# Kernel optimization log

Measured on AMD Instinct MI355X. Metric: run time of the kernel, lower is better.

Reference implementation:

```python
import jax, jax.numpy as jnp
import numpy as np

B, S, T, E, H, V = 32, 64, 64, 512, 512, 32000  # batch, src len, tgt len, embed, hidden(per dir), vocab


def _lstm_scan(xs, Wih, Whh, bih, bhh, h0, c0):
    # xs: [S, B, E]; PyTorch gate order i, f, g, o
    def step(carry, x):
        h, c = carry
        g = x @ Wih.T + bih + h @ Whh.T + bhh
        i, f, gg, o = jnp.split(g, 4, axis=-1)
        c = jax.nn.sigmoid(f) * c + jax.nn.sigmoid(i) * jnp.tanh(gg)
        h = jax.nn.sigmoid(o) * jnp.tanh(c)
        return (h, c), h
    (hT, cT), hs = jax.lax.scan(step, (h0, c0), xs)
    return hs, hT, cT


def setup_inputs() -> dict:
    key = jax.random.key(0)
    ks = jax.random.split(key, 20)
    p = lambda k, shape, s=0.05: (jax.random.normal(k, shape, jnp.float32) * s)
    inp = {
        "input_chunk": jax.random.randint(ks[0], (B, S), 0, V),
        "target_chunk": jax.random.randint(ks[1], (B, T), 0, V),
        "enc_emb": jax.random.uniform(ks[2], (V, E), jnp.float32, -0.1, 0.1),
        "dec_emb": jax.random.uniform(ks[3], (V, E), jnp.float32, -0.1, 0.1),
        # encoder bidirectional LSTM (1 layer)
        "Wih_f": p(ks[4], (4 * H, E)), "Whh_f": p(ks[5], (4 * H, H)),
        "bih_f": p(ks[6], (4 * H,)), "bhh_f": p(ks[7], (4 * H,)),
        "Wih_b": p(ks[8], (4 * H, E)), "Whh_b": p(ks[9], (4 * H, H)),
        "bih_b": p(ks[10], (4 * H,)), "bhh_b": p(ks[11], (4 * H,)),
        # decoder LSTMCell: input 2H+E, hidden 2H
        "Wih_d": p(ks[12], (8 * H, 2 * H + E)), "Whh_d": p(ks[13], (8 * H, 2 * H)),
        "bih_d": p(ks[14], (8 * H,)), "bhh_d": p(ks[15], (8 * H,)),
        # attention projection 2H -> 2H
        "Wa": p(ks[16], (2 * H, 2 * H)), "ba": p(ks[17], (2 * H,)),
        # output projection 2H -> V (bias initialized to 0 in the module)
        "Wout": p(ks[18], (V, 2 * H)), "bout": jnp.zeros((V,), jnp.float32),
    }
    return inp


def reference(input_chunk, target_chunk, enc_emb, dec_emb,
              Wih_f, Whh_f, bih_f, bhh_f, Wih_b, Whh_b, bih_b, bhh_b,
              Wih_d, Whh_d, bih_d, bhh_d, Wa, ba, Wout, bout):
    # ---- Encoder: bidirectional LSTM ----
    x = enc_emb[input_chunk]                 # [B, S, E]
    xs = jnp.transpose(x, (1, 0, 2))         # [S, B, E]
    h0 = jnp.zeros((B, H), x.dtype)
    c0 = jnp.zeros((B, H), x.dtype)
    hs_f, hT_f, cT_f = _lstm_scan(xs, Wih_f, Whh_f, bih_f, bhh_f, h0, c0)
    hs_b, hT_b, cT_b = _lstm_scan(xs[::-1], Wih_b, Whh_b, bih_b, bhh_b, h0, c0)
    hs_b = hs_b[::-1]
    all_hidden = jnp.concatenate([hs_f, hs_b], axis=-1)          # [S, B, 2H]
    all_hidden = jnp.transpose(all_hidden, (1, 0, 2))            # [B, S, 2H]
    dec_h = jnp.concatenate([hT_f, hT_b], axis=-1)               # [B, 2H]
    dec_c = jnp.concatenate([cT_f, cT_b], axis=-1)               # [B, 2H]

    # ---- Decoder: attention + LSTMCell loop (teacher forcing = 1.0, no dropout) ----
    A = all_hidden @ Wa.T + ba               # W_attention(all_hidden), constant across steps
    tgt_emb = dec_emb[target_chunk]          # [B, T, E]
    # feed at t=0 is zeros; afterwards the t-th target embedding
    feeds = jnp.concatenate([jnp.zeros((B, 1, E), tgt_emb.dtype), tgt_emb[:, :-1]], axis=1)
    feeds = jnp.transpose(feeds, (1, 0, 2))  # [T, B, E]

    def dstep(carry, feed):
        h, c = carry
        scores = jnp.einsum('bsd,bd->bs', A, h)                  # [B, S]
        attn = jax.nn.softmax(scores, axis=1)
        ctx = jnp.einsum('bs,bsd->bd', attn, all_hidden)         # [B, 2H]
        inp = jnp.concatenate([ctx, feed], axis=1)               # [B, 2H+E]
        g = inp @ Wih_d.T + bih_d + h @ Whh_d.T + bhh_d
        i, f, gg, o = jnp.split(g, 4, axis=-1)
        c = jax.nn.sigmoid(f) * c + jax.nn.sigmoid(i) * jnp.tanh(gg)
        h = jax.nn.sigmoid(o) * jnp.tanh(c)
        logits = h @ Wout.T + bout                               # [B, V]
        return (h, c), logits

    _, logits = jax.lax.scan(dstep, (dec_h, dec_c), feeds)       # [T, B, V]
    logits = jnp.transpose(logits, (1, 0, 2))                    # [B, T, V]
    outputs = jnp.argmax(logits, axis=-1)                        # [B, T]
    return logits, outputs
```

## Files before the change

### kernel.cpp

```cpp
#include <hip/hip_runtime.h>
#include <hip/hip_bf16.h>

#define BB 32
#define SS 64
#define TT 64
#define EE 512
#define HH 512
#define VV 32000

#define O_C0    0u
#define O_C1    32768u
#define O_HD    65536u
#define O_CD    98304u
#define O_PENC  131072u
#define O_PDEC  655360u
#define O_CTX   1179648u
#define O_ALLH  1212416u
#define O_AATT  3309568u
#define O_HDEC  5406720u
#define O_PACK  7503872u
#define O_DA1   7507968u
#define O_DA2   7540736u
#define O_W1    7573504u
#define WS_NEED 95830016ull

#define S_GXF   0u
#define S_GXB   4194304u
#define S_GFEED 8388608u
#define U_BASE  17000000u

typedef float f32x4 __attribute__((ext_vector_type(4)));
typedef _Float16 f16x8 __attribute__((ext_vector_type(8)));
typedef _Float16 f16x4 __attribute__((ext_vector_type(4)));

__device__ __forceinline__ float sigm_(float x){ return 1.0f/(1.0f + expf(-x)); }

__device__ __forceinline__ unsigned int fkey_(float f){
  unsigned int u = __float_as_uint(f);
  return (u & 0x80000000u) ? ~u : (u | 0x80000000u);
}

__device__ __forceinline__ int swz_(int row, int kb){
  return (row*64 + kb) ^ ((row & 7) << 4);
}
__device__ __forceinline__ int swz128_(int row, int kb){
  return (row*128 + kb) ^ ((row & 7) << 4);
}

__global__ __launch_bounds__(256) void k_init(float* __restrict__ ws){
  int i = blockIdx.x*256 + threadIdx.x;
  if (i < 65536) ws[i] = 0.0f;
  if (i < 2048) ((unsigned long long*)(ws + O_PACK))[i] = 0ull;
}

__global__ __launch_bounds__(256) void k_cvtW(
    const float* __restrict__ Whh_f, const float* __restrict__ Whh_b,
    const float* __restrict__ Wih_d, const float* __restrict__ Whh_d,
    _Float16* __restrict__ dst)
{
  int g = blockIdx.x*256 + threadIdx.x;
  int idx = g*4;
  f32x4 v;
  if (idx < 1048576){
    v = *(const f32x4*)(Whh_f + idx);
  } else if (idx < 2097152){
    v = *(const f32x4*)(Whh_b + (idx - 1048576));
  } else {
    int j = idx - 2097152;
    int row = j >> 11, col = j & 2047;
    const float* src = (col < 1024) ? (Wih_d + (size_t)row*1536 + col)
                                    : (Whh_d + (size_t)row*1024 + (col - 1024));
    v = *(const f32x4*)src;
  }
  f16x4 h;
  #pragma unroll
  for (int c = 0; c < 4; ++c) h[c] = (_Float16)v[c];
  *(f16x4*)(dst + idx) = h;
}

__global__ __launch_bounds__(256) void k_cvtWout(
    const float* __restrict__ Wout, _Float16* __restrict__ W1)
{
  size_t i = ((size_t)blockIdx.x*256 + threadIdx.x)*8;
  f32x4 x0 = *(const f32x4*)(Wout + i);
  f32x4 x1 = *(const f32x4*)(Wout + i + 4);
  f16x4 h0, h1;
  #pragma unroll
  for (int c = 0; c < 4; ++c){ h0[c] = (_Float16)x0[c]; h1[c] = (_Float16)x1[c]; }
  *(f16x4*)(W1 + i)   = h0;
  *(f16x4*)(W1 + i+4) = h1;
}

template<int MODE>
__global__ __launch_bounds__(256) void k_gemm(
    const float* __restrict__ A, int lda,
    const int* __restrict__ chunk,
    const float* __restrict__ W, int ldW,
    const float* __restrict__ bias0, const float* __restrict__ bias1,
    float* __restrict__ C, int ldC, int K)
{
  __shared__ float As[16*68];
  __shared__ float Bs[16*68];
  int tid = threadIdx.x;
  int n0 = blockIdx.x*64, m0 = blockIdx.y*64;
  int tx = tid & 15, ty = tid >> 4;
  int lrow = tid >> 2, kq = tid & 3;

  const float* arp;
  if (MODE == 0) {
    arp = A + (size_t)(m0 + lrow)*lda;
  } else if (MODE == 1) {
    int m = m0 + lrow; int s = m >> 5, b = m & 31;
    arp = A + (size_t)chunk[b*SS + s]*EE;
  } else {
    int m = m0 + lrow; int t = m >> 5, b = m & 31;
    arp = (t == 0) ? nullptr : A + (size_t)chunk[b*TT + (t-1)]*EE;
  }
  const float* wrp = W + (size_t)(n0 + lrow)*ldW;

  float acc[4][4] = {};
  for (int k0 = 0; k0 < K; k0 += 16){
    float4 va = make_float4(0.f,0.f,0.f,0.f);
    if (MODE == 0) va = *(const float4*)&arp[k0 + kq*4];
    else if (arp)  va = *(const float4*)&arp[k0 + kq*4];
    float4 vw = *(const float4*)&wrp[k0 + kq*4];
    As[(kq*4+0)*68 + lrow] = va.x;
    As[(kq*4+1)*68 + lrow] = va.y;
    As[(kq*4+2)*68 + lrow] = va.z;
    As[(kq*4+3)*68 + lrow] = va.w;
    Bs[(kq*4+0)*68 + lrow] = vw.x;
    Bs[(kq*4+1)*68 + lrow] = vw.y;
    Bs[(kq*4+2)*68 + lrow] = vw.z;
    Bs[(kq*4+3)*68 + lrow] = vw.w;
    __syncthreads();
    #pragma unroll
    for (int kk = 0; kk < 16; ++kk){
      float4 a4 = *(const float4*)&As[kk*68 + ty*4];
      float4 b4 = *(const float4*)&Bs[kk*68 + tx*4];
      float av[4] = {a4.x,a4.y,a4.z,a4.w};
      float bv[4] = {b4.x,b4.y,b4.z,b4.w};
      #pragma unroll
      for (int i=0;i<4;++i)
        #pragma unroll
        for (int j=0;j<4;++j)
          acc[i][j] = fmaf(av[i], bv[j], acc[i][j]);
    }
    __syncthreads();
  }
  float bv[4];
  #pragma unroll
  for (int j = 0; j < 4; ++j){
    int n = n0 + tx*4 + j;
    float bb = 0.f;
    if (bias0) bb += bias0[n];
    if (bias1) bb += bias1[n];
    bv[j] = bb;
  }
  #pragma unroll
  for (int i = 0; i < 4; ++i){
    int m = m0 + ty*4 + i;
    float4 v = make_float4(acc[i][0]+bv[0], acc[i][1]+bv[1], acc[i][2]+bv[2], acc[i][3]+bv[3]);
    *(float4*)&C[(size_t)m*ldC + n0 + tx*4] = v;
  }
}

__global__ __launch_bounds__(256) void k_enc_step(
    const _Float16* __restrict__ wenc,
    float* __restrict__ ws, const float* __restrict__ oscr, int t)
{
  __shared__ float hl[128*36];
  __shared__ float Wt[32*132];
  int sub = blockIdx.x, kp = blockIdx.y, dir = blockIdx.z;
  int tid = threadIdx.x;
  int s = dir ? (63 - t) : t;
  int p = t & 1;
  const float* gx  = oscr + (dir ? S_GXB : S_GXF);
  const float* prd = ws + (p ? O_PDEC : O_PENC) + dir*262144u;
  const float* cin = ws + O_C0 + p*32768u + dir*16384u;
  float* cout = ws + O_C0 + (p^1)*32768u + dir*16384u;

  {
    int ug = tid & 31, bg = tid >> 5;
    int ul0 = ug*4;
    int u0 = kp*128 + ul0;
    #pragma unroll
    for (int j = 0; j < 4; ++j){
      int b = bg*4 + j;
      size_t gbase = (size_t)(s*32 + b)*2048u;
      f32x4 g0 = *(const f32x4*)&gx[gbase + u0];
      f32x4 g1 = *(const f32x4*)&gx[gbase + 512 + u0];
      f32x4 g2 = *(const f32x4*)&gx[gbase + 1024 + u0];
      f32x4 g3 = *(const f32x4*)&gx[gbase + 1536 + u0];
      if (t > 0){
        #pragma unroll
        for (int kq = 0; kq < 4; ++kq){
          const float* pp = prd + kq*65536u + (size_t)b*2048u;
          g0 += *(const f32x4*)&pp[u0];
          g1 += *(const f32x4*)&pp[512 + u0];
          g2 += *(const f32x4*)&pp[1024 + u0];
          g3 += *(const f32x4*)&pp[1536 + u0];
        }
      }
      f32x4 c = *(const f32x4*)&cin[b*512 + u0];
      f32x4 cn, hn;
      #pragma unroll
      for (int e = 0; e < 4; ++e){
        float cc = sigm_(g1[e])*c[e] + sigm_(g0[e])*tanhf(g2[e]);
        float hh = sigm_(g3[e])*tanhf(cc);
        cn[e] = cc; hn[e] = hh;
        hl[(ul0+e)*36 + b] = hh;
      }
      if (sub == 0){
        *(f32x4*)&cout[b*512 + u0] = cn;
        *(f32x4*)&ws[O_ALLH + (size_t)(b*64 + s)*1024u + dir*512 + u0] = hn;
      }
    }
  }
  __syncthreads();
  if (t == 63) return;

  const _Float16* W = wenc + dir*1048576u;
  float* P = ws + (p ? O_PENC : O_PDEC) + dir*262144u + kp*65536u;
  int rg2 = tid & 31, bg2 = tid >> 5;
  int wrow = tid & 127, whalf = tid >> 7;
  float acc[4][4] = {};
  for (int kt = 0; kt < 4; ++kt){
    #pragma unroll
    for (int i = 0; i < 4; ++i){
      int chunk = whalf*4 + i;
      int grow = sub*128 + wrow;
      f16x4 v = *(const f16x4*)&W[(size_t)grow*512 + kp*128 + kt*32 + chunk*4];
      Wt[(chunk*4+0)*132 + wrow] = (float)v[0];
      Wt[(chunk*4+1)*132 + wrow] = (float)v[1];
      Wt[(chunk*4+2)*132 + wrow] = (float)v[2];
      Wt[(chunk*4+3)*132 + wrow] = (float)v[3];
    }
    __syncthreads();
    #pragma unroll 8
    for (int kk = 0; kk < 32; ++kk){
      f32x4 wv = *(const f32x4*)&Wt[kk*132 + rg2*4];
      f32x4 hv = *(const f32x4*)&hl[(kt*32+kk)*36 + bg2*4];
      #pragma unroll
      for (int i = 0; i < 4; ++i)
        #pragma unroll
        for (int j = 0; j < 4; ++j)
          acc[i][j] = fmaf(wv[i], hv[j], acc[i][j]);
    }
    __syncthreads();
  }
  #pragma unroll
  for (int j = 0; j < 4; ++j){
    int b = bg2*4 + j;
    f32x4 v; v[0]=acc[0][j]; v[1]=acc[1][j]; v[2]=acc[2][j]; v[3]=acc[3][j];
    *(f32x4*)&P[(size_t)b*2048u + sub*128 + rg2*4] = v;
  }
}

__global__ __launch_bounds__(256) void k_concat(float* __restrict__ ws){
  int i = blockIdx.x*256 + threadIdx.x;
  int which = i >> 15;
  int idx = i & 32767;
  int b = idx >> 10, u = idx & 1023;
  int dir = (u >= 512);
  int uu = u & 511;
  float v;
  if (which == 0){
    int s = dir ? 0 : 63;
    v = ws[O_ALLH + (size_t)(b*64 + s)*1024u + u];
  } else {
    v = ws[O_C0 + dir*16384u + b*512 + uu];
  }
  ws[(which ? O_CD : O_HD) + b*1024 + u] = v;
}

__global__ __launch_bounds__(256) void k_attn(float* __restrict__ ws,
                                              const float* __restrict__ oscr, int t){
  __shared__ float hlq[1024];
  __shared__ float part[64][5];
  __shared__ float sc[64];
  __shared__ float atn[64];
  __shared__ float dsh;
  int b = blockIdx.x, tid = threadIdx.x;
  float* hd = ws + O_HD;
  float* cd = ws + O_CD;
  float* G  = ws + O_PDEC;
  _Float16* DA1 = (_Float16*)(ws + O_DA1);
  _Float16* DA2 = (_Float16*)(ws + O_DA2);
  if (t > 0){
    const float* gfd = oscr + S_GFEED + (size_t)((t-1)*32 + b)*4096u;
    for (int u = tid; u < 1024; u += 256){
      float g0 = gfd[u]      + G[(size_t)b*4096u + u];
      float g1 = gfd[1024+u] + G[(size_t)b*4096u + 1024 + u];
      float g2 = gfd[2048+u] + G[(size_t)b*4096u + 2048 + u];
      float g3 = gfd[3072+u] + G[(size_t)b*4096u + 3072 + u];
      float c = cd[b*1024 + u];
      c = sigm_(g1)*c + sigm_(g0)*tanhf(g2);
      float h = sigm_(g3)*tanhf(c);
      cd[b*1024+u] = c; hd[b*1024+u] = h; hlq[u] = h;
      ws[O_HDEC + (size_t)(b*64 + (t-1))*1024u + u] = h;
      _Float16 hi = (_Float16)h;
      DA1[(size_t)b*2048u + 1024 + u] = hi;
      DA2[(size_t)b*2048u + 1024 + u] = (_Float16)((h - (float)hi)*2048.0f);
    }
  } else {
    for (int u = tid; u < 1024; u += 256){
      float h = hd[b*1024 + u];
      hlq[u] = h;
      _Float16 hi = (_Float16)h;
      DA1[(size_t)b*2048u + 1024 + u] = hi;
      DA2[(size_t)b*2048u + 1024 + u] = (_Float16)((h - (float)hi)*2048.0f);
    }
  }
  __syncthreads();
  {
    int s = tid >> 2, p = tid & 3;
    const float* Ar = ws + O_AATT + (size_t)(b*64 + s)*1024u + p*256;
    const float* hp = &hlq[p*256];
    float sum = 0.f;
    #pragma unroll 8
    for (int k4 = 0; k4 < 64; ++k4){
      float4 a = *(const float4*)&Ar[k4*4];
      float4 h4 = *(const float4*)&hp[k4*4];
      sum = fmaf(a.x,h4.x, fmaf(a.y,h4.y, fmaf(a.z,h4.z, fmaf(a.w,h4.w, sum))));
    }
    part[s][p] = sum;
  }
  __syncthreads();
  if (tid < 64) sc[tid] = part[tid][0] + part[tid][1] + part[tid][2] + part[tid][3];
  __syncthreads();
  if (tid < 64){
    float m = sc[0];
    #pragma unroll
    for (int i = 1; i < 64; ++i) m = fmaxf(m, sc[i]);
    atn[tid] = expf(sc[tid] - m);
  }
  __syncthreads();
  if (tid == 0){
    float d = 0.f;
    #pragma unroll
    for (int i = 0; i < 64; ++i) d += atn[i];
    dsh = 1.0f/d;
  }
  __syncthreads();
  {
    float rd = dsh;
    float ax=0.f, ay=0.f, az=0.f, aw=0.f;
    const float* ah = ws + O_ALLH + (size_t)(b*64)*1024u + tid*4;
    for (int s2 = 0; s2 < 64; ++s2){
      float a = atn[s2];
      float4 v = *(const float4*)&ah[(size_t)s2*1024u];
      ax = fmaf(a, v.x, ax); ay = fmaf(a, v.y, ay);
      az = fmaf(a, v.z, az); aw = fmaf(a, v.w, aw);
    }
    float o[4] = {ax*rd, ay*rd, az*rd, aw*rd};
    #pragma unroll
    for (int j = 0; j < 4; ++j){
      int u = tid*4 + j;
      _Float16 hi = (_Float16)o[j];
      DA1[(size_t)b*2048u + u] = hi;
      DA2[(size_t)b*2048u + u] = (_Float16)((o[j] - (float)hi)*2048.0f);
    }
  }
}

__global__ __launch_bounds__(256) void k_dec_gemm(
    const _Float16* __restrict__ wdec, float* __restrict__ ws)
{
  __shared__ char glds[24576];
  int bid = blockIdx.x, tid = threadIdx.x;
  float* G = ws + O_PDEC;
  const _Float16* DA1 = (const _Float16*)(ws + O_DA1);
  const _Float16* DA2 = (const _Float16*)(ws + O_DA2);
  const float rs = 1.0f/2048.0f;
  int lane = tid & 63, w = tid >> 6;
  int lr = lane & 15, lg = lane >> 4;
  int mfw = w >> 1, nfw = w & 1;
  int arow = tid >> 3, aseg = tid & 7;
  const _Float16* a1src = DA1 + (size_t)arow*2048u + aseg*8;
  const _Float16* a2src = DA2 + (size_t)arow*2048u + aseg*8;
  const _Float16* wsrc  = wdec + (size_t)(bid*32 + arow)*2048u + aseg*8;
  f32x4 accH, accM;
  accH[0]=accH[1]=accH[2]=accH[3]=0.f;
  accM[0]=accM[1]=accM[2]=accM[3]=0.f;
  uint4 rA1 = *(const uint4*)a1src;
  uint4 rA2 = *(const uint4*)a2src;
  uint4 rW  = *(const uint4*)wsrc;
  int so = swz128_(arow, aseg*16);
  int raA = swz128_(mfw*16 + lr, lg*16);
  int raW = swz128_(nfw*16 + lr, lg*16);
  for (int kt = 0; kt < 32; ++kt){
    char* base = glds + (kt & 1)*12288;
    char* A1t = base; char* A2t = base + 4096; char* Wt = base + 8192;
    *(uint4*)(A1t + so) = rA1;
    *(uint4*)(A2t + so) = rA2;
    *(uint4*)(Wt  + so) = rW;
    __syncthreads();
    if (kt < 31){
      int ko = (kt+1)*64;
      rA1 = *(const uint4*)(a1src + ko);
      rA2 = *(const uint4*)(a2src + ko);
      rW  = *(const uint4*)(wsrc + ko);
    }
    #pragma unroll
    for (int ks = 0; ks < 2; ++ks){
      f16x8 a1 = *(const f16x8*)(A1t + (raA ^ (ks*64)));
      f16x8 a2 = *(const f16x8*)(A2t + (raA ^ (ks*64)));
      f16x8 wf = *(const f16x8*)(Wt  + (raW ^ (ks*64)));
      accH = __builtin_amdgcn_mfma_f32_16x16x32_f16(a1, wf, accH, 0, 0, 0);
      accM = __builtin_amdgcn_mfma_f32_16x16x32_f16(a2, wf, accM, 0, 0, 0);
    }
    __syncthreads();
  }
  #pragma unroll
  for (int r = 0; r < 4; ++r){
    int b = mfw*16 + lg*4 + r;
    int n = bid*32 + nfw*16 + lr;
    G[(size_t)b*4096u + n] = accH[r] + accM[r]*rs;
  }
}

__global__ __launch_bounds__(256) void k_dec_pw_last(float* __restrict__ ws,
                                                     const float* __restrict__ oscr){
  int g = blockIdx.x*256 + threadIdx.x;
  int b = g >> 10, u = g & 1023;
  const float* gfd = oscr + S_GFEED + (size_t)(63*32 + b)*4096u;
  const float* G = ws + O_PDEC;
  float g0 = gfd[u]      + G[(size_t)b*4096u + u];
  float g1 = gfd[1024+u] + G[(size_t)b*4096u + 1024 + u];
  float g2 = gfd[2048+u] + G[(size_t)b*4096u + 2048 + u];
  float g3 = gfd[3072+u] + G[(size_t)b*4096u + 3072 + u];
  float c = ws[O_CD + b*1024 + u];
  c = sigm_(g1)*c + sigm_(g0)*tanhf(g2);
  float h = sigm_(g3)*tanhf(c);
  ws[O_HDEC + (size_t)(b*64 + 63)*1024u + u] = h;
}

__global__ __launch_bounds__(256) void k_cvtA(float* __restrict__ ws){
  const float* src = ws + O_HDEC;
  _Float16* A1 = (_Float16*)(ws + O_ALLH);
  _Float16* A2 = (_Float16*)(ws + O_AATT);
  int i = (blockIdx.x*256 + threadIdx.x)*8;
  f32x4 x0 = *(const f32x4*)&src[i];
  f32x4 x1 = *(const f32x4*)&src[i+4];
  f16x4 h0, h1, l0, l1;
  #pragma unroll
  for (int c = 0; c < 4; ++c){
    _Float16 a = (_Float16)x0[c];
    h0[c] = a; l0[c] = (_Float16)((x0[c] - (float)a)*2048.0f);
    _Float16 bq = (_Float16)x1[c];
    h1[c] = bq; l1[c] = (_Float16)((x1[c] - (float)bq)*2048.0f);
  }
  *(f16x4*)&A1[i]   = h0;
  *(f16x4*)&A1[i+4] = h1;
  *(f16x4*)&A2[i]   = l0;
  *(f16x4*)&A2[i+4] = l1;
}

__global__ __launch_bounds__(256) void k_logits(
    const _Float16* __restrict__ A1, const _Float16* __restrict__ A2,
    const _Float16* __restrict__ W1, const float* __restrict__ bout,
    float* __restrict__ out, unsigned long long* __restrict__ pk)
{
  __shared__ char lds[49152];
  int tid = threadIdx.x;
  int n0 = blockIdx.y*128, m0 = blockIdx.x*128;
  int lane = tid & 63, wave = tid >> 6;
  int wm = wave >> 1, wn = wave & 1;
  int lr = lane & 15, lg = lane >> 4;

  int s0 = tid*2, s1 = tid*2 + 1;
  int ar0 = s0 >> 2, as0 = s0 & 3;
  int ar1 = s1 >> 2, as1 = s1 & 3;
  const _Float16* a1p0 = A1 + (size_t)(m0 + ar0)*1024u + as0*8;
  const _Float16* a1p1 = A1 + (size_t)(m0 + ar1)*1024u + as1*8;
  const _Float16* a2p0 = A2 + (size_t)(m0 + ar0)*1024u + as0*8;
  const _Float16* a2p1 = A2 + (size_t)(m0 + ar1)*1024u + as1*8;
  const _Float16* wp0  = W1 + (size_t)(n0 + ar0)*1024u + as0*8;
  const _Float16* wp1  = W1 + (size_t)(n0 + ar1)*1024u + as1*8;

  f32x4 accH[4][4], accM[4][4];
  #pragma unroll
  for (int i = 0; i < 4; ++i)
    #pragma unroll
    for (int j = 0; j < 4; ++j){
      f32x4 z; z[0]=z[1]=z[2]=z[3]=0.f;
      accH[i][j] = z; accM[i][j] = z;
    }

  uint4 r10, r11, r20, r21, rw0, rw1;
  r10 = *(const uint4*)a1p0; r11 = *(const uint4*)a1p1;
  r20 = *(const uint4*)a2p0; r21 = *(const uint4*)a2p1;
  rw0 = *(const uint4*)wp0;  rw1 = *(const uint4*)wp1;

  for (int kt = 0; kt < 32; ++kt){
    int cur = kt & 1;
    char* base = lds + cur*24576;
    char* A1t = base, *A2t = base + 8192, *Wt = base + 16384;
    *(uint4*)(A1t + swz_(ar0, as0*16)) = r10;
    *(uint4*)(A1t + swz_(ar1, as1*16)) = r11;
    *(uint4*)(A2t + swz_(ar0, as0*16)) = r20;
    *(uint4*)(A2t + swz_(ar1, as1*16)) = r21;
    *(uint4*)(Wt  + swz_(ar0, as0*16)) = rw0;
    *(uint4*)(Wt  + swz_(ar1, as1*16)) = rw1;
    __syncthreads();
    if (kt < 31){
      int ko = (kt+1)*32;
      r10 = *(const uint4*)(a1p0 + ko); r11 = *(const uint4*)(a1p1 + ko);
      r20 = *(const uint4*)(a2p0 + ko); r21 = *(const uint4*)(a2p1 + ko);
      rw0 = *(const uint4*)(wp0 + ko);  rw1 = *(const uint4*)(wp1 + ko);
    }
    f16x8 wf[4];
    #pragma unroll
    for (int nf = 0; nf < 4; ++nf)
      wf[nf] = *(const f16x8*)(Wt + swz_(wn*64 + nf*16 + lr, lg*16));
    #pragma unroll
    for (int mf = 0; mf < 4; ++mf){
      int ad = swz_(wm*64 + mf*16 + lr, lg*16);
      f16x8 a1f = *(const f16x8*)(A1t + ad);
      f16x8 a2f = *(const f16x8*)(A2t + ad);
      #pragma unroll
      for (int nf = 0; nf < 4; ++nf){
        accH[mf][nf] = __builtin_amdgcn_mfma_f32_16x16x32_f16(a1f, wf[nf], accH[mf][nf], 0, 0, 0);
        accM[mf][nf] = __builtin_amdgcn_mfma_f32_16x16x32_f16(a2f, wf[nf], accM[mf][nf], 0, 0, 0);
      }
    }
    __syncthreads();
  }

  const float rs = 1.0f/2048.0f;
  float bb[4];
  #pragma unroll
  for (int nf = 0; nf < 4; ++nf) bb[nf] = bout[n0 + wn*64 + nf*16 + lr];
  #pragma unroll
  for (int mf = 0; mf < 4; ++mf){
    #pragma unroll
    for (int r = 0; r < 4; ++r){
      int m = m0 + wm*64 + mf*16 + lg*4 + r;
      unsigned long long bk = 0ull;
      #pragma unroll
      for (int nf = 0; nf < 4; ++nf){
        int n = n0 + wn*64 + nf*16 + lr;
        float val = accH[mf][nf][r] + accM[mf][nf][r]*rs + bb[nf];
        __builtin_nontemporal_store(val, &out[(size_t)m*VV + n]);
        unsigned long long p = ((unsigned long long)fkey_(val) << 32) | (unsigned int)(~(unsigned int)n);
        if (p > bk) bk = p;
      }
      #pragma unroll
      for (int off = 1; off < 16; off <<= 1){
        unsigned long long o = __shfl_xor(bk, off, 64);
        if (o > bk) bk = o;
      }
      if (lr == 0) atomicMax(&pk[m], bk);
    }
  }
}

__global__ __launch_bounds__(512) void k_logits_fb(
    const _Float16* __restrict__ A1, const _Float16* __restrict__ A2,
    const float* __restrict__ Wout, const float* __restrict__ bout,
    float* __restrict__ out, unsigned long long* __restrict__ pk)
{
  __shared__ char lds[49152];
  char* A1t = lds;
  char* A2t = lds + 8192;
  char* W1t = lds + 16384;
  char* W2t = lds + 32768;
  int tid = threadIdx.x;
  int n0 = blockIdx.x*256;
  int lane = tid & 63, wave = tid >> 6;
  int wm = wave >> 2, wn = wave & 3;
  int lr = lane & 15, lg = lane >> 4;

  int arow = tid >> 2, aseg = tid & 3;
  int wrow = tid >> 1, wseg = tid & 1;
  const float* wp = Wout + (size_t)(n0 + wrow)*1024u + wseg*16;

  float bb[4];
  #pragma unroll
  for (int nf = 0; nf < 4; ++nf) bb[nf] = bout[n0 + wn*64 + nf*16 + lr];
  const float rs = 1.0f/2048.0f;

  for (int mi = 0; mi < 4; ++mi){
    int m0 = (blockIdx.y*4 + mi)*128;
    const _Float16* a1p = A1 + (size_t)(m0 + arow)*1024u + aseg*8;
    const _Float16* a2p = A2 + (size_t)(m0 + arow)*1024u + aseg*8;

    f32x4 accH[4][4], accM[4][4];
    #pragma unroll
    for (int i = 0; i < 4; ++i)
      #pragma unroll
      for (int j = 0; j < 4; ++j){
        f32x4 z; z[0]=z[1]=z[2]=z[3]=0.f;
        accH[i][j] = z; accM[i][j] = z;
      }

    for (int k0 = 0; k0 < 1024; k0 += 32){
      uint4 av1 = *(const uint4*)(a1p + k0);
      uint4 av2 = *(const uint4*)(a2p + k0);
      f32x4 wv[4];
      #pragma unroll
      for (int i = 0; i < 4; ++i) wv[i] = *(const f32x4*)(wp + k0 + i*4);
      __syncthreads();
      *(uint4*)(A1t + swz_(arow, aseg*16)) = av1;
      *(uint4*)(A2t + swz_(arow, aseg*16)) = av2;
      f16x8 hi[2], lo[2];
      #pragma unroll
      for (int i = 0; i < 2; ++i)
        #pragma unroll
        for (int c = 0; c < 8; ++c){
          float x = wv[i*2 + (c>>2)][c&3];
          _Float16 h = (_Float16)x;
          hi[i][c] = h;
          lo[i][c] = (_Float16)((x - (float)h)*2048.0f);
        }
      *(f16x8*)(W1t + swz_(wrow, wseg*32 +  0)) = hi[0];
      *(f16x8*)(W1t + swz_(wrow, wseg*32 + 16)) = hi[1];
      *(f16x8*)(W2t + swz_(wrow, wseg*32 +  0)) = lo[0];
      *(f16x8*)(W2t + swz_(wrow, wseg*32 + 16)) = lo[1];
      __syncthreads();
      f16x8 w1f[4], w2f[4];
      #pragma unroll
      for (int nf = 0; nf < 4; ++nf){
        int ad = swz_(wn*64 + nf*16 + lr, lg*16);
        w1f[nf] = *(const f16x8*)(W1t + ad);
        w2f[nf] = *(const f16x8*)(W2t + ad);
      }
      #pragma unroll
      for (int mf = 0; mf < 4; ++mf){
        int ad = swz_(wm*64 + mf*16 + lr, lg*16);
        f16x8 a1f = *(const f16x8*)(A1t + ad);
        f16x8 a2f = *(const f16x8*)(A2t + ad);
        #pragma unroll
        for (int nf = 0; nf < 4; ++nf){
          accH[mf][nf] = __builtin_amdgcn_mfma_f32_16x16x32_f16(a1f, w1f[nf], accH[mf][nf], 0, 0, 0);
          accM[mf][nf] = __builtin_amdgcn_mfma_f32_16x16x32_f16(a1f, w2f[nf], accM[mf][nf], 0, 0, 0);
          accM[mf][nf] = __builtin_amdgcn_mfma_f32_16x16x32_f16(a2f, w1f[nf], accM[mf][nf], 0, 0, 0);
        }
      }
    }

    #pragma unroll
    for (int mf = 0; mf < 4; ++mf){
      #pragma unroll
      for (int r = 0; r < 4; ++r){
        int m = m0 + wm*64 + mf*16 + lg*4 + r;
        unsigned long long bk = 0ull;
        #pragma unroll
        for (int nf = 0; nf < 4; ++nf){
          int n = n0 + wn*64 + nf*16 + lr;
          float val = accH[mf][nf][r] + accM[mf][nf][r]*rs + bb[nf];
          __builtin_nontemporal_store(val, &out[(size_t)m*VV + n]);
          unsigned long long p = ((unsigned long long)fkey_(val) << 32) | (unsigned int)(~(unsigned int)n);
          if (p > bk) bk = p;
        }
        #pragma unroll
        for (int off = 1; off < 16; off <<= 1){
          unsigned long long o = __shfl_xor(bk, off, 64);
          if (o > bk) bk = o;
        }
        if (lr == 0) atomicMax(&pk[m], bk);
      }
    }
  }
}

__global__ __launch_bounds__(256) void k_argmax(
    const unsigned long long* __restrict__ pk, float* __restrict__ out)
{
  int i = blockIdx.x*256 + threadIdx.x;
  if (i < 2048){
    unsigned int low = (unsigned int)(pk[i] & 0xFFFFFFFFull);
    unsigned int col = ~low;
    out[(size_t)BB*TT*VV + i] = (float)col;
  }
}

extern "C" void kernel_launch(void* const* d_in, const int* in_sizes, int n_in,
                              void* d_out, int out_size, void* d_ws, size_t ws_size,
                              hipStream_t stream)
{
  const int*   input_chunk  = (const int*)d_in[0];
  const int*   target_chunk = (const int*)d_in[1];
  const float* enc_emb = (const float*)d_in[2];
  const float* dec_emb = (const float*)d_in[3];
  const float* Wih_f = (const float*)d_in[4];
  const float* Whh_f = (const float*)d_in[5];
  const float* bih_f = (const float*)d_in[6];
  const float* bhh_f = (const float*)d_in[7];
  const float* Wih_b = (const float*)d_in[8];
  const float* Whh_b = (const float*)d_in[9];
  const float* bih_b = (const float*)d_in[10];
  const float* bhh_b = (const float*)d_in[11];
  const float* Wih_d = (const float*)d_in[12];
  const float* Whh_d = (const float*)d_in[13];
  const float* bih_d = (const float*)d_in[14];
  const float* bhh_d = (const float*)d_in[15];
  const float* Wa   = (const float*)d_in[16];
  const float* ba   = (const float*)d_in[17];
  const float* Wout = (const float*)d_in[18];
  const float* bout = (const float*)d_in[19];
  float* ws = (float*)d_ws;
  float* out = (float*)d_out;
  float* oscr = (float*)d_out;
  _Float16* wf16 = (_Float16*)(oscr + U_BASE);
  bool bigws = (ws_size >= WS_NEED);

  k_init<<<256, 256, 0, stream>>>(ws);
  k_cvtW<<<10240, 256, 0, stream>>>(Whh_f, Whh_b, Wih_d, Whh_d, wf16);
  if (bigws)
    k_cvtWout<<<16000, 256, 0, stream>>>(Wout, (_Float16*)(ws + O_W1));

  k_gemm<1><<<dim3(32,32), 256, 0, stream>>>(enc_emb, 512, input_chunk, Wih_f, 512, bih_f, bhh_f, oscr + S_GXF, 2048, 512);
  k_gemm<1><<<dim3(32,32), 256, 0, stream>>>(enc_emb, 512, input_chunk, Wih_b, 512, bih_b, bhh_b, oscr + S_GXB, 2048, 512);
  k_gemm<2><<<dim3(64,32), 256, 0, stream>>>(dec_emb, 512, target_chunk, Wih_d + 1024, 1536, bih_d, bhh_d, oscr + S_GFEED, 4096, 512);

  for (int t = 0; t < 64; ++t){
    k_enc_step<<<dim3(16,4,2), 256, 0, stream>>>(wf16, ws, oscr, t);
  }

  k_concat<<<256, 256, 0, stream>>>(ws);
  k_gemm<0><<<dim3(16,32), 256, 0, stream>>>(ws + O_ALLH, 1024, nullptr, Wa, 1024, ba, nullptr, ws + O_AATT, 1024, 1024);

  const _Float16* wdec = wf16 + 2097152u;
  for (int t = 0; t < 64; ++t){
    k_attn<<<32, 256, 0, stream>>>(ws, oscr, t);
    k_dec_gemm<<<128, 256, 0, stream>>>(wdec, ws);
  }
  k_dec_pw_last<<<128, 256, 0, stream>>>(ws, oscr);

  k_cvtA<<<1024, 256, 0, stream>>>(ws);
  if (bigws){
    k_logits<<<dim3(16,250), 256, 0, stream>>>(
        (const _Float16*)(ws + O_ALLH), (const _Float16*)(ws + O_AATT),
        (const _Float16*)(ws + O_W1), bout, out, (unsigned long long*)(ws + O_PACK));
  } else {
    k_logits_fb<<<dim3(125,4), 512, 0, stream>>>(
        (const _Float16*)(ws + O_ALLH), (const _Float16*)(ws + O_AATT),
        Wout, bout, out, (unsigned long long*)(ws + O_PACK));
  }
  k_argmax<<<8, 256, 0, stream>>>((const unsigned long long*)(ws + O_PACK), out);
}
```

Before: 4.064 ms.

## Move encoder recurrent GEMM to split-fp16 MFMA and drop LDS staging in decoder GEMM

```diff
diff --git a/kernel.cpp b/kernel.cpp
--- a/kernel.cpp
+++ b/kernel.cpp
@@ -9,7 +9,6 @@
 #define VV 32000
 
 #define O_C0    0u
-#define O_C1    32768u
 #define O_HD    65536u
 #define O_CD    98304u
 #define O_PENC  131072u
@@ -43,13 +42,10 @@
 __device__ __forceinline__ int swz_(int row, int kb){
   return (row*64 + kb) ^ ((row & 7) << 4);
 }
-__device__ __forceinline__ int swz128_(int row, int kb){
-  return (row*128 + kb) ^ ((row & 7) << 4);
-}
 
 __global__ __launch_bounds__(256) void k_init(float* __restrict__ ws){
   int i = blockIdx.x*256 + threadIdx.x;
-  if (i < 65536) ws[i] = 0.0f;
+  if (i < 131072) ws[i] = 0.0f;
   if (i < 2048) ((unsigned long long*)(ws + O_PACK))[i] = 0ull;
 }
 
@@ -168,92 +164,97 @@
     const _Float16* __restrict__ wenc,
     float* __restrict__ ws, const float* __restrict__ oscr, int t)
 {
-  __shared__ float hl[128*36];
-  __shared__ float Wt[32*132];
-  int sub = blockIdx.x, kp = blockIdx.y, dir = blockIdx.z;
+  __shared__ _Float16 hA1[32][520];
+  __shared__ _Float16 hA2[32][520];
+  int nb = blockIdx.x, dir = blockIdx.y;
   int tid = threadIdx.x;
   int s = dir ? (63 - t) : t;
   int p = t & 1;
   const float* gx  = oscr + (dir ? S_GXB : S_GXF);
-  const float* prd = ws + (p ? O_PDEC : O_PENC) + dir*262144u;
+  const float* Gin = ws + O_PENC + (size_t)(p*2 + dir)*65536u;
+  float* Gout      = ws + O_PENC + (size_t)((p^1)*2 + dir)*65536u;
   const float* cin = ws + O_C0 + p*32768u + dir*16384u;
-  float* cout = ws + O_C0 + (p^1)*32768u + dir*16384u;
-
-  {
-    int ug = tid & 31, bg = tid >> 5;
-    int ul0 = ug*4;
-    int u0 = kp*128 + ul0;
-    #pragma unroll
-    for (int j = 0; j < 4; ++j){
-      int b = bg*4 + j;
-      size_t gbase = (size_t)(s*32 + b)*2048u;
-      f32x4 g0 = *(const f32x4*)&gx[gbase + u0];
-      f32x4 g1 = *(const f32x4*)&gx[gbase + 512 + u0];
-      f32x4 g2 = *(const f32x4*)&gx[gbase + 1024 + u0];
-      f32x4 g3 = *(const f32x4*)&gx[gbase + 1536 + u0];
-      if (t > 0){
-        #pragma unroll
-        for (int kq = 0; kq < 4; ++kq){
-          const float* pp = prd + kq*65536u + (size_t)b*2048u;
-          g0 += *(const f32x4*)&pp[u0];
-          g1 += *(const f32x4*)&pp[512 + u0];
-          g2 += *(const f32x4*)&pp[1024 + u0];
-          g3 += *(const f32x4*)&pp[1536 + u0];
-        }
-      }
-      f32x4 c = *(const f32x4*)&cin[b*512 + u0];
-      f32x4 cn, hn;
-      #pragma unroll
-      for (int e = 0; e < 4; ++e){
-        float cc = sigm_(g1[e])*c[e] + sigm_(g0[e])*tanhf(g2[e]);
-        float hh = sigm_(g3[e])*tanhf(cc);
-        cn[e] = cc; hn[e] = hh;
-        hl[(ul0+e)*36 + b] = hh;
-      }
-      if (sub == 0){
-        *(f32x4*)&cout[b*512 + u0] = cn;
-        *(f32x4*)&ws[O_ALLH + (size_t)(b*64 + s)*1024u + dir*512 + u0] = hn;
-      }
+  float* cout      = ws + O_C0 + (p^1)*32768u + dir*16384u;
+
+  #pragma unroll
+  for (int j = 0; j < 16; ++j){
+    int item = tid + j*256;
+    int b = item >> 7, u0 = (item & 127)*4;
+    size_t gb = (size_t)(s*32 + b)*2048u + u0;
+    f32x4 g0 = *(const f32x4*)&gx[gb];
+    f32x4 g1 = *(const f32x4*)&gx[gb + 512];
+    f32x4 g2 = *(const f32x4*)&gx[gb + 1024];
+    f32x4 g3 = *(const f32x4*)&gx[gb + 1536];
+    if (t > 0){
+      int o = b*2048 + u0;
+      g0 += *(const f32x4*)&Gin[o];
+      g1 += *(const f32x4*)&Gin[o + 512];
+      g2 += *(const f32x4*)&Gin[o + 1024];
+      g3 += *(const f32x4*)&Gin[o + 1536];
+    }
+    f32x4 c = *(const f32x4*)&cin[b*512 + u0];
+    f32x4 cn, hn;
+    f16x4 h1v, h2v;
+    #pragma unroll
+    for (int e = 0; e < 4; ++e){
+      float cc = sigm_(g1[e])*c[e] + sigm_(g0[e])*tanhf(g2[e]);
+      float hh = sigm_(g3[e])*tanhf(cc);
+      cn[e] = cc; hn[e] = hh;
+      _Float16 hi = (_Float16)hh;
+      h1v[e] = hi;
+      h2v[e] = (_Float16)((hh - (float)hi)*2048.0f);
+    }
+    *(f16x4*)&hA1[b][u0] = h1v;
+    *(f16x4*)&hA2[b][u0] = h2v;
+    if (nb == 0){
+      *(f32x4*)&cout[b*512 + u0] = cn;
+      *(f32x4*)&ws[O_ALLH + (size_t)(b*64 + s)*1024u + dir*512 + u0] = hn;
     }
   }
   __syncthreads();
   if (t == 63) return;
 
-  const _Float16* W = wenc + dir*1048576u;
-  float* P = ws + (p ? O_PENC : O_PDEC) + dir*262144u + kp*65536u;
-  int rg2 = tid & 31, bg2 = tid >> 5;
-  int wrow = tid & 127, whalf = tid >> 7;
-  float acc[4][4] = {};
-  for (int kt = 0; kt < 4; ++kt){
-    #pragma unroll
-    for (int i = 0; i < 4; ++i){
-      int chunk = whalf*4 + i;
-      int grow = sub*128 + wrow;
-      f16x4 v = *(const f16x4*)&W[(size_t)grow*512 + kp*128 + kt*32 + chunk*4];
-      Wt[(chunk*4+0)*132 + wrow] = (float)v[0];
-      Wt[(chunk*4+1)*132 + wrow] = (float)v[1];
-      Wt[(chunk*4+2)*132 + wrow] = (float)v[2];
-      Wt[(chunk*4+3)*132 + wrow] = (float)v[3];
-    }
-    __syncthreads();
-    #pragma unroll 8
-    for (int kk = 0; kk < 32; ++kk){
-      f32x4 wv = *(const f32x4*)&Wt[kk*132 + rg2*4];
-      f32x4 hv = *(const f32x4*)&hl[(kt*32+kk)*36 + bg2*4];
-      #pragma unroll
-      for (int i = 0; i < 4; ++i)
-        #pragma unroll
-        for (int j = 0; j < 4; ++j)
-          acc[i][j] = fmaf(wv[i], hv[j], acc[i][j]);
-    }
-    __syncthreads();
-  }
-  #pragma unroll
-  for (int j = 0; j < 4; ++j){
-    int b = bg2*4 + j;
-    f32x4 v; v[0]=acc[0][j]; v[1]=acc[1][j]; v[2]=acc[2][j]; v[3]=acc[3][j];
-    *(f32x4*)&P[(size_t)b*2048u + sub*128 + rg2*4] = v;
-  }
+  const _Float16* W = wenc + (size_t)dir*1048576u;
+  int lane = tid & 63, w = tid >> 6;
+  int lr = lane & 15, lg = lane >> 4;
+  int n0g = nb*256 + w*64;
+  f32x4 accH[2][4], accM[2][4];
+  #pragma unroll
+  for (int i = 0; i < 2; ++i)
+    #pragma unroll
+    for (int j = 0; j < 4; ++j){
+      f32x4 z; z[0]=z[1]=z[2]=z[3]=0.f;
+      accH[i][j] = z; accM[i][j] = z;
+    }
+  for (int kt = 0; kt < 16; ++kt){
+    int koff = kt*32 + lg*8;
+    f16x8 a1f[2], a2f[2];
+    #pragma unroll
+    for (int mf = 0; mf < 2; ++mf){
+      a1f[mf] = *(const f16x8*)&hA1[mf*16 + lr][koff];
+      a2f[mf] = *(const f16x8*)&hA2[mf*16 + lr][koff];
+    }
+    #pragma unroll
+    for (int nf = 0; nf < 4; ++nf){
+      f16x8 wf = *(const f16x8*)&W[(size_t)(n0g + nf*16 + lr)*512u + koff];
+      #pragma unroll
+      for (int mf = 0; mf < 2; ++mf){
+        accH[mf][nf] = __builtin_amdgcn_mfma_f32_16x16x32_f16(a1f[mf], wf, accH[mf][nf], 0, 0, 0);
+        accM[mf][nf] = __builtin_amdgcn_mfma_f32_16x16x32_f16(a2f[mf], wf, accM[mf][nf], 0, 0, 0);
+      }
+    }
+  }
+  const float rs = 1.0f/2048.0f;
+  #pragma unroll
+  for (int mf = 0; mf < 2; ++mf)
+    #pragma unroll
+    for (int nf = 0; nf < 4; ++nf)
+      #pragma unroll
+      for (int r = 0; r < 4; ++r){
+        int b = mf*16 + lg*4 + r;
+        int n = n0g + nf*16 + lr;
+        Gout[b*2048 + n] = accH[mf][nf][r] + accM[mf][nf][r]*rs;
+      }
 }
 
 __global__ __launch_bounds__(256) void k_concat(float* __restrict__ ws){
@@ -366,55 +367,33 @@
 __global__ __launch_bounds__(256) void k_dec_gemm(
     const _Float16* __restrict__ wdec, float* __restrict__ ws)
 {
-  __shared__ char glds[24576];
   int bid = blockIdx.x, tid = threadIdx.x;
   float* G = ws + O_PDEC;
   const _Float16* DA1 = (const _Float16*)(ws + O_DA1);
   const _Float16* DA2 = (const _Float16*)(ws + O_DA2);
-  const float rs = 1.0f/2048.0f;
   int lane = tid & 63, w = tid >> 6;
   int lr = lane & 15, lg = lane >> 4;
-  int mfw = w >> 1, nfw = w & 1;
-  int arow = tid >> 3, aseg = tid & 7;
-  const _Float16* a1src = DA1 + (size_t)arow*2048u + aseg*8;
-  const _Float16* a2src = DA2 + (size_t)arow*2048u + aseg*8;
-  const _Float16* wsrc  = wdec + (size_t)(bid*32 + arow)*2048u + aseg*8;
+  int mf = w >> 1, nf = w & 1;
+  const _Float16* a1row = DA1 + (size_t)(mf*16 + lr)*2048u;
+  const _Float16* a2row = DA2 + (size_t)(mf*16 + lr)*2048u;
+  const _Float16* wrow  = wdec + (size_t)(bid*32 + nf*16 + lr)*2048u;
   f32x4 accH, accM;
   accH[0]=accH[1]=accH[2]=accH[3]=0.f;
   accM[0]=accM[1]=accM[2]=accM[3]=0.f;
-  uint4 rA1 = *(const uint4*)a1src;
-  uint4 rA2 = *(const uint4*)a2src;
-  uint4 rW  = *(const uint4*)wsrc;
-  int so = swz128_(arow, aseg*16);
-  int raA = swz128_(mfw*16 + lr, lg*16);
-  int raW = swz128_(nfw*16 + lr, lg*16);
-  for (int kt = 0; kt < 32; ++kt){
-    char* base = glds + (kt & 1)*12288;
-    char* A1t = base; char* A2t = base + 4096; char* Wt = base + 8192;
-    *(uint4*)(A1t + so) = rA1;
-    *(uint4*)(A2t + so) = rA2;
-    *(uint4*)(Wt  + so) = rW;
-    __syncthreads();
-    if (kt < 31){
-      int ko = (kt+1)*64;
-      rA1 = *(const uint4*)(a1src + ko);
-      rA2 = *(const uint4*)(a2src + ko);
-      rW  = *(const uint4*)(wsrc + ko);
-    }
-    #pragma unroll
-    for (int ks = 0; ks < 2; ++ks){
-      f16x8 a1 = *(const f16x8*)(A1t + (raA ^ (ks*64)));
-      f16x8 a2 = *(const f16x8*)(A2t + (raA ^ (ks*64)));
-      f16x8 wf = *(const f16x8*)(Wt  + (raW ^ (ks*64)));
-      accH = __builtin_amdgcn_mfma_f32_16x16x32_f16(a1, wf, accH, 0, 0, 0);
-      accM = __builtin_amdgcn_mfma_f32_16x16x32_f16(a2, wf, accM, 0, 0, 0);
-    }
-    __syncthreads();
-  }
+  #pragma unroll 4
+  for (int kt = 0; kt < 64; ++kt){
+    int koff = kt*32 + lg*8;
+    f16x8 a1 = *(const f16x8*)(a1row + koff);
+    f16x8 a2 = *(const f16x8*)(a2row + koff);
+    f16x8 wf = *(const f16x8*)(wrow + koff);
+    accH = __builtin_amdgcn_mfma_f32_16x16x32_f16(a1, wf, accH, 0, 0, 0);
+    accM = __builtin_amdgcn_mfma_f32_16x16x32_f16(a2, wf, accM, 0, 0, 0);
+  }
+  const float rs = 1.0f/2048.0f;
   #pragma unroll
   for (int r = 0; r < 4; ++r){
-    int b = mfw*16 + lg*4 + r;
-    int n = bid*32 + nfw*16 + lr;
+    int b = mf*16 + lg*4 + r;
+    int n = bid*32 + nf*16 + lr;
     G[(size_t)b*4096u + n] = accH[r] + accM[r]*rs;
   }
 }
@@ -705,7 +684,7 @@
   _Float16* wf16 = (_Float16*)(oscr + U_BASE);
   bool bigws = (ws_size >= WS_NEED);
 
-  k_init<<<256, 256, 0, stream>>>(ws);
+  k_init<<<512, 256, 0, stream>>>(ws);
   k_cvtW<<<10240, 256, 0, stream>>>(Whh_f, Whh_b, Wih_d, Whh_d, wf16);
   if (bigws)
     k_cvtWout<<<16000, 256, 0, stream>>>(Wout, (_Float16*)(ws + O_W1));
@@ -715,7 +694,7 @@
   k_gemm<2><<<dim3(64,32), 256, 0, stream>>>(dec_emb, 512, target_chunk, Wih_d + 1024, 1536, bih_d, bhh_d, oscr + S_GFEED, 4096, 512);
 
   for (int t = 0; t < 64; ++t){
-    k_enc_step<<<dim3(16,4,2), 256, 0, stream>>>(wf16, ws, oscr, t);
+    k_enc_step<<<dim3(8,2), 256, 0, stream>>>(wf16, ws, oscr, t);
   }
 
   k_concat<<<256, 256, 0, stream>>>(ws);
```

New measurement: 5.778 ms. 1.42x slower.
